# Kernel optimization log

Hardware: AMD Instinct MI355X
Metric: run time of the kernel (lower is better)

The kernel has to match this reference:

```python
import jax, jax.numpy as jnp
import numpy as np

N = 50000      # nodes
E = 800000     # edges (avg degree 16)
D = 128        # node_embedding_dim
H = 256        # hidden_dim


def setup_inputs() -> dict:
    key = jax.random.key(0)
    ks = jax.random.split(key, 12)
    init = lambda k, shape, fan: (jax.random.normal(k, shape, jnp.float32) / np.sqrt(fan).astype(np.float32))
    return {
        "node_ids": jnp.arange(N, dtype=jnp.int32),
        "edge_index": jax.random.randint(ks[0], (2, E), 0, N, jnp.int32),
        "neighbour_edge_index": jax.random.randint(ks[1], (2, E), 0, N, jnp.int32),
        "edge_attr": jax.random.uniform(ks[2], (E,), jnp.float32),
        "emb": init(ks[3], (N, D), D),          # Embedding table
        "W_in": init(ks[4], (D, H), D), "b_in": jnp.zeros((H,), jnp.float32),
        "W_out": init(ks[5], (H, D), H), "b_out": jnp.zeros((D,), jnp.float32),
        "W1": init(ks[6], (2 * D, D), 2 * D), "b1": jnp.zeros((D,), jnp.float32),
        "W2": init(ks[7], (D, D), D), "b2": jnp.zeros((D,), jnp.float32),
        "W3": init(ks[8], (D, 1), D), "b3": jnp.zeros((1,), jnp.float32),
    }


def gcn_conv(x, W, b, edge_index, w):
    """PyG GCNConv, add_self_loops=False, normalize=True.
    out_i = b + sum_{(j->i)} d_i^{-1/2} w_ji d_j^{-1/2} (x_j @ W)
    deg_i = sum of incoming edge weights at target node i.
    """
    row, col = edge_index[0], edge_index[1]
    deg = jax.ops.segment_sum(w, col, num_segments=N)
    dinv = jnp.where(deg > 0, 1.0 / jnp.sqrt(deg), 0.0)
    norm = dinv[row] * w * dinv[col]                    # [E]
    h = x @ W                                           # [N, out]
    msg = h[row] * norm[:, None]                        # [E, out]
    return jax.ops.segment_sum(msg, col, num_segments=N) + b


def reference(node_ids, edge_index, neighbour_edge_index, edge_attr,
              emb, W_in, b_in, W_out, b_out, W1, b1, W2, b2, W3, b3):
    x = emb[node_ids]                                   # embedding lookup [N, D]
    x = jax.nn.elu(gcn_conv(x, W_in, b_in, edge_index, edge_attr))
    ones = jnp.ones((neighbour_edge_index.shape[1],), x.dtype)
    x = jax.nn.elu(gcn_conv(x, W_out, b_out, neighbour_edge_index, ones))
    # edge-level gather-concat-MLP decoder
    src, dst = edge_index[0], edge_index[1]
    h = jnp.concatenate([x[src], x[dst]], axis=1)       # [E, 2D]
    h = jax.nn.relu(h @ W1 + b1)
    h = jax.nn.relu(h @ W2 + b2)
    return (h @ W3 + b3).squeeze(-1)                    # [E]
```

## Files before the change

kernel.cpp:

```cpp
#include <hip/hip_runtime.h>
#include <math.h>

#define NN 50000
#define NE 800000

typedef __attribute__((ext_vector_type(8))) short s8_t;
typedef __attribute__((ext_vector_type(4))) float f4_t;

__device__ __forceinline__ short bf16_rne(float v) {
  unsigned u = __float_as_uint(v);
  unsigned r = (u + 0x7FFFu + ((u >> 16) & 1u)) >> 16;
  return (short)r;
}
__device__ __forceinline__ float bf16_tof(short h) {
  return __uint_as_float(((unsigned)(unsigned short)h) << 16);
}
__device__ __forceinline__ void split2(float v, short& hi, short& lo) {
  hi = bf16_rne(v);
  lo = bf16_rne(v - bf16_tof(hi));
}


__global__ __launch_bounds__(256) void k_wcvt(const float* __restrict__ W1,
                                              const float* __restrict__ W2,
                                              short* __restrict__ w1th,
                                              short* __restrict__ w1tl,
                                              short* __restrict__ w2th,
                                              short* __restrict__ w2tl) {
  int i = blockIdx.x * 256 + threadIdx.x;
  if (i < 32768) {
    int k = i >> 7, n = i & 127;
    short h, l; split2(W1[i], h, l);
    w1th[n * 256 + k] = h; w1tl[n * 256 + k] = l;
  } else if (i < 49152) {
    int j = i - 32768;
    int k = j >> 7, n = j & 127;
    short h, l; split2(W2[j], h, l);
    w2th[n * 128 + k] = h; w2tl[n * 128 + k] = l;
  }
}


__global__ __launch_bounds__(256) void k_hist(const int* __restrict__ ei,
                                              const int* __restrict__ nei,
                                              const float* __restrict__ w,
                                              int* __restrict__ cnt1,
                                              float* __restrict__ deg1,
                                              int* __restrict__ cnt2) {
  int e = blockIdx.x * 256 + threadIdx.x;
  if (e < NE) {
    int c1 = ei[NE + e];
    atomicAdd(&cnt1[c1], 1);
    atomicAdd(&deg1[c1], w[e]);
    atomicAdd(&cnt2[nei[NE + e]], 1);
  }
}

__global__ __launch_bounds__(256) void k_dinvs(const float* __restrict__ deg1,
                                               const int* __restrict__ cnt2,
                                               float* __restrict__ dinv1,
                                               float* __restrict__ dinv2) {
  int i = blockIdx.x * 256 + threadIdx.x;
  if (i < NN) {
    float d1 = deg1[i];
    dinv1[i] = d1 > 0.f ? (1.0f / sqrtf(d1)) : 0.f;
    int c2 = cnt2[i];
    dinv2[i] = c2 > 0 ? (1.0f / sqrtf((float)c2)) : 0.f;
  }
}


#define NCHUNK 196

__global__ __launch_bounds__(256) void k_scan_part(const int* __restrict__ cnt1,
                                                   const int* __restrict__ cnt2,
                                                   int* __restrict__ part) {
  int g = blockIdx.x >= NCHUNK;
  int chunk = g ? blockIdx.x - NCHUNK : blockIdx.x;
  const int* cnt = g ? cnt2 : cnt1;
  int i = chunk * 256 + threadIdx.x;
  int v = (i < NN) ? cnt[i] : 0;
  __shared__ int sd[4];
#pragma unroll
  for (int o = 32; o; o >>= 1) v += __shfl_down(v, o);
  if ((threadIdx.x & 63) == 0) sd[threadIdx.x >> 6] = v;
  __syncthreads();
  if (threadIdx.x == 0) part[blockIdx.x] = sd[0] + sd[1] + sd[2] + sd[3];
}

__global__ __launch_bounds__(256) void k_scan_mid(int* __restrict__ part,
                                                  int* __restrict__ off1_last,
                                                  int* __restrict__ off2_last) {
  __shared__ int sd[256];
  for (int g = 0; g < 2; g++) {
    int base = g * NCHUNK;
    int v = (threadIdx.x < NCHUNK) ? part[base + threadIdx.x] : 0;
    sd[threadIdx.x] = v;
    __syncthreads();
    for (int o = 1; o < 256; o <<= 1) {
      int x = (threadIdx.x >= o) ? sd[threadIdx.x - o] : 0;
      __syncthreads();
      sd[threadIdx.x] += x;
      __syncthreads();
    }
    if (threadIdx.x < NCHUNK) part[base + threadIdx.x] = sd[threadIdx.x] - v;
    if (threadIdx.x == 255) *(g ? off2_last : off1_last) = sd[255];
    __syncthreads();
  }
}

__global__ __launch_bounds__(256) void k_scan_final(const int* __restrict__ cnt1,
                                                    const int* __restrict__ cnt2,
                                                    const int* __restrict__ part,
                                                    int* __restrict__ off1,
                                                    int* __restrict__ pos1,
                                                    int* __restrict__ off2,
                                                    int* __restrict__ pos2) {
  int g = blockIdx.x >= NCHUNK;
  int chunk = g ? blockIdx.x - NCHUNK : blockIdx.x;
  const int* cnt = g ? cnt2 : cnt1;
  int* off = g ? off2 : off1;
  int* pos = g ? pos2 : pos1;
  __shared__ int sd[256];
  int i = chunk * 256 + threadIdx.x;
  int v = (i < NN) ? cnt[i] : 0;
  sd[threadIdx.x] = v;
  __syncthreads();
  for (int o = 1; o < 256; o <<= 1) {
    int x = (threadIdx.x >= o) ? sd[threadIdx.x - o] : 0;
    __syncthreads();
    sd[threadIdx.x] += x;
    __syncthreads();
  }
  if (i < NN) {
    int ex = part[blockIdx.x] + sd[threadIdx.x] - v;
    off[i] = ex; pos[i] = ex;
  }
}


__global__ __launch_bounds__(256) void k_fill(const int* __restrict__ ei,
                                              const int* __restrict__ nei,
                                              const float* __restrict__ w,
                                              const float* __restrict__ dinv1,
                                              const float* __restrict__ dinv2,
                                              int* __restrict__ pos1,
                                              int* __restrict__ csr1_src,
                                              float* __restrict__ csr1_nrm,
                                              int* __restrict__ csr1_dst,
                                              int* __restrict__ csr1_eid,
                                              int* __restrict__ pos2,
                                              int* __restrict__ csr2_src,
                                              float* __restrict__ csr2_nrm) {
  int e = blockIdx.x * 256 + threadIdx.x;
  if (e < NE) {
    int r = ei[e], c = ei[NE + e];
    float nv = dinv1[r] * w[e] * dinv1[c];
    int s = atomicAdd(&pos1[c], 1);
    csr1_src[s] = r; csr1_nrm[s] = nv; csr1_dst[s] = c; csr1_eid[s] = e;
    int r2 = nei[e], c2 = nei[NE + e];
    float nv2 = dinv2[r2] * dinv2[c2];
    int s2 = atomicAdd(&pos2[c2], 1);
    csr2_src[s2] = r2; csr2_nrm[s2] = nv2;
  }
}


__global__ __launch_bounds__(256) void k_agg1(const int* __restrict__ off,
                                              const int* __restrict__ csr_src,
                                              const float* __restrict__ csr_nrm,
                                              const int* __restrict__ ids,
                                              const float* __restrict__ emb,
                                              float* __restrict__ aggX) {
  int wave = threadIdx.x >> 6, lane = threadIdx.x & 63;
  int node = blockIdx.x * 4 + wave;
  int start = off[node], end = off[node + 1];
  float2 acc = make_float2(0.f, 0.f);
  int i = start;
  for (; i + 3 < end; i += 4) {
    int s0 = csr_src[i], s1 = csr_src[i + 1], s2 = csr_src[i + 2], s3 = csr_src[i + 3];
    float n0 = csr_nrm[i], n1 = csr_nrm[i + 1], n2 = csr_nrm[i + 2], n3 = csr_nrm[i + 3];
    float2 v0 = *(const float2*)(emb + (size_t)ids[s0] * 128 + lane * 2);
    float2 v1 = *(const float2*)(emb + (size_t)ids[s1] * 128 + lane * 2);
    float2 v2 = *(const float2*)(emb + (size_t)ids[s2] * 128 + lane * 2);
    float2 v3 = *(const float2*)(emb + (size_t)ids[s3] * 128 + lane * 2);
    acc.x = fmaf(n0, v0.x, fmaf(n1, v1.x, fmaf(n2, v2.x, fmaf(n3, v3.x, acc.x))));
    acc.y = fmaf(n0, v0.y, fmaf(n1, v1.y, fmaf(n2, v2.y, fmaf(n3, v3.y, acc.y))));
  }
  for (; i < end; i++) {
    int s0 = csr_src[i];
    float n0 = csr_nrm[i];
    float2 v0 = *(const float2*)(emb + (size_t)ids[s0] * 128 + lane * 2);
    acc.x = fmaf(n0, v0.x, acc.x);
    acc.y = fmaf(n0, v0.y, acc.y);
  }
  *(float2*)(aggX + (size_t)node * 128 + lane * 2) = acc;
}


__global__ __launch_bounds__(256) void k_agg2(const int* __restrict__ off,
                                              const int* __restrict__ csr_src,
                                              const float* __restrict__ csr_nrm,
                                              const float* __restrict__ h2,
                                              const float* __restrict__ b,
                                              short* __restrict__ xh,
                                              short* __restrict__ xl) {
  int wave = threadIdx.x >> 6, lane = threadIdx.x & 63;
  int node = blockIdx.x * 4 + wave;
  int start = off[node], end = off[node + 1];
  float2 acc = make_float2(0.f, 0.f);
  int i = start;
  for (; i + 3 < end; i += 4) {
    int s0 = csr_src[i], s1 = csr_src[i + 1], s2 = csr_src[i + 2], s3 = csr_src[i + 3];
    float n0 = csr_nrm[i], n1 = csr_nrm[i + 1], n2 = csr_nrm[i + 2], n3 = csr_nrm[i + 3];
    float2 v0 = *(const float2*)(h2 + (size_t)s0 * 128 + lane * 2);
    float2 v1 = *(const float2*)(h2 + (size_t)s1 * 128 + lane * 2);
    float2 v2 = *(const float2*)(h2 + (size_t)s2 * 128 + lane * 2);
    float2 v3 = *(const float2*)(h2 + (size_t)s3 * 128 + lane * 2);
    acc.x = fmaf(n0, v0.x, fmaf(n1, v1.x, fmaf(n2, v2.x, fmaf(n3, v3.x, acc.x))));
    acc.y = fmaf(n0, v0.y, fmaf(n1, v1.y, fmaf(n2, v2.y, fmaf(n3, v3.y, acc.y))));
  }
  for (; i < end; i++) {
    int s0 = csr_src[i];
    float n0 = csr_nrm[i];
    float2 v0 = *(const float2*)(h2 + (size_t)s0 * 128 + lane * 2);
    acc.x = fmaf(n0, v0.x, acc.x);
    acc.y = fmaf(n0, v0.y, acc.y);
  }
  float vx = acc.x + b[lane * 2];
  float vy = acc.y + b[lane * 2 + 1];
  vx = vx > 0.f ? vx : expm1f(vx);
  vy = vy > 0.f ? vy : expm1f(vy);
  short hx, lx, hy, ly;
  split2(vx, hx, lx);
  split2(vy, hy, ly);
  unsigned hp = (unsigned)(unsigned short)hx | ((unsigned)(unsigned short)hy << 16);
  unsigned lp = (unsigned)(unsigned short)lx | ((unsigned)(unsigned short)ly << 16);
  *(unsigned*)(xh + (size_t)node * 128 + lane * 2) = hp;
  *(unsigned*)(xl + (size_t)node * 128 + lane * 2) = lp;
}


__global__ __launch_bounds__(256) void k_gemm_aggin(const float* __restrict__ X,
                                                    const float* __restrict__ W,
                                                    const float* __restrict__ b,
                                                    float* __restrict__ C) {
  __shared__ float As[32][128];
  int r0 = blockIdx.x * 32;
  int t = threadIdx.x;
  for (int i = t; i < 1024; i += 256) {
    int r = i >> 5, q = (i & 31) << 2;
    int rr = r0 + r;
    float4 v = make_float4(0.f, 0.f, 0.f, 0.f);
    if (rr < NN) v = *(const float4*)(X + (size_t)rr * 128 + q);
    *(float4*)(&As[r][q]) = v;
  }
  __syncthreads();
  int tc = t & 31, tr = t >> 5;
  int c0 = tc * 8, rr0 = tr * 4;
  float acc[4][8];
#pragma unroll
  for (int r = 0; r < 4; r++)
#pragma unroll
    for (int c = 0; c < 8; c++) acc[r][c] = 0.f;

  for (int k0 = 0; k0 < 128; k0 += 4) {
    float a_[4][4];
#pragma unroll
    for (int r = 0; r < 4; r++) {
      float4 v = *(const float4*)(&As[rr0 + r][k0]);
      a_[r][0] = v.x; a_[r][1] = v.y; a_[r][2] = v.z; a_[r][3] = v.w;
    }
#pragma unroll
    for (int kk = 0; kk < 4; kk++) {
      float4 w0 = *(const float4*)(W + (size_t)(k0 + kk) * 256 + c0);
      float4 w1 = *(const float4*)(W + (size_t)(k0 + kk) * 256 + c0 + 4);
#pragma unroll
      for (int r = 0; r < 4; r++) {
        float av = a_[r][kk];
        acc[r][0] += av * w0.x; acc[r][1] += av * w0.y;
        acc[r][2] += av * w0.z; acc[r][3] += av * w0.w;
        acc[r][4] += av * w1.x; acc[r][5] += av * w1.y;
        acc[r][6] += av * w1.z; acc[r][7] += av * w1.w;
      }
    }
  }
  float4 bb0 = *(const float4*)(b + c0);
  float4 bb1 = *(const float4*)(b + c0 + 4);
#pragma unroll
  for (int r = 0; r < 4; r++) {
    int rr = r0 + rr0 + r;
    if (rr < NN) {
      float o[8];
      o[0] = acc[r][0] + bb0.x; o[1] = acc[r][1] + bb0.y;
      o[2] = acc[r][2] + bb0.z; o[3] = acc[r][3] + bb0.w;
      o[4] = acc[r][4] + bb1.x; o[5] = acc[r][5] + bb1.y;
      o[6] = acc[r][6] + bb1.z; o[7] = acc[r][7] + bb1.w;
#pragma unroll
      for (int c = 0; c < 8; c++) o[c] = o[c] > 0.f ? o[c] : expm1f(o[c]);
      *(float4*)(C + (size_t)rr * 256 + c0) = make_float4(o[0], o[1], o[2], o[3]);
      *(float4*)(C + (size_t)rr * 256 + c0 + 4) = make_float4(o[4], o[5], o[6], o[7]);
    }
  }
}


__global__ __launch_bounds__(256) void k_gemm_mid(const float* __restrict__ X,
                                                  const float* __restrict__ W,
                                                  float* __restrict__ C) {
  __shared__ float As[32][256];
  int r0 = blockIdx.x * 32;
  int t = threadIdx.x;
  for (int i = t; i < 2048; i += 256) {
    int r = i >> 6, q = (i & 63) << 2;
    int rr = r0 + r;
    float4 v = make_float4(0.f, 0.f, 0.f, 0.f);
    if (rr < NN) v = *(const float4*)(X + (size_t)rr * 256 + q);
    *(float4*)(&As[r][q]) = v;
  }
  __syncthreads();
  int tc = t & 31, tr = t >> 5;
  int c0 = tc * 4, rr0 = tr * 4;
  float acc[4][4];
#pragma unroll
  for (int r = 0; r < 4; r++)
#pragma unroll
    for (int c = 0; c < 4; c++) acc[r][c] = 0.f;

  for (int k0 = 0; k0 < 256; k0 += 4) {
    float a_[4][4];
#pragma unroll
    for (int r = 0; r < 4; r++) {
      float4 v = *(const float4*)(&As[rr0 + r][k0]);
      a_[r][0] = v.x; a_[r][1] = v.y; a_[r][2] = v.z; a_[r][3] = v.w;
    }
#pragma unroll
    for (int kk = 0; kk < 4; kk++) {
      float4 w = *(const float4*)(W + (size_t)(k0 + kk) * 128 + c0);
#pragma unroll
      for (int r = 0; r < 4; r++) {
        float av = a_[r][kk];
        acc[r][0] += av * w.x; acc[r][1] += av * w.y;
        acc[r][2] += av * w.z; acc[r][3] += av * w.w;
      }
    }
  }
#pragma unroll
  for (int r = 0; r < 4; r++) {
    int rr = r0 + rr0 + r;
    if (rr < NN) {
      float4 o = make_float4(acc[r][0], acc[r][1], acc[r][2], acc[r][3]);
      *(float4*)(C + (size_t)rr * 128 + c0) = o;
    }
  }
}


__global__ __launch_bounds__(256) void k_pab(const short* __restrict__ x2h,
                                             const short* __restrict__ x2l,
                                             const short* __restrict__ w1th,
                                             const short* __restrict__ w1tl,
                                             const float* __restrict__ b1,
                                             float* __restrict__ Pa,
                                             float* __restrict__ Pb) {
  __shared__ short Xh[32 * 136];
  __shared__ short Xl[32 * 136];
  int t = threadIdx.x;
  int n0 = blockIdx.x * 32;
#pragma unroll
  for (int j = 0; j < 2; j++) {
    int i = t + 256 * j;
    int row = i >> 4, q = i & 15;
    int node = n0 + row; if (node >= NN) node = NN - 1;
    *(uint4*)&Xh[row * 136 + q * 8] = *(const uint4*)(x2h + (size_t)node * 128 + q * 8);
    *(uint4*)&Xl[row * 136 + q * 8] = *(const uint4*)(x2l + (size_t)node * 128 + q * 8);
  }
  __syncthreads();

  int w = t >> 6, lane = t & 63;
  int quad = lane >> 4, l16 = lane & 15;
  int nb = w * 32;
  int aoff0 = l16 * 136 + quad * 8;
  int aoff1 = (16 + l16) * 136 + quad * 8;
  int bo0 = (nb + l16) * 256 + quad * 8;
  int bo1 = (nb + 16 + l16) * 256 + quad * 8;

  f4_t aa[2][2], ab[2][2];
#pragma unroll
  for (int mi = 0; mi < 2; mi++)
#pragma unroll
    for (int ni = 0; ni < 2; ni++) {
      aa[mi][ni] = (f4_t){0.f, 0.f, 0.f, 0.f};
      ab[mi][ni] = (f4_t){0.f, 0.f, 0.f, 0.f};
    }

#pragma unroll
  for (int kb = 0; kb < 4; kb++) {
    int k0 = kb * 32;
    s8_t ah0 = *(const s8_t*)&Xh[aoff0 + k0];
    s8_t ah1 = *(const s8_t*)&Xh[aoff1 + k0];
    s8_t al0 = *(const s8_t*)&Xl[aoff0 + k0];
    s8_t al1 = *(const s8_t*)&Xl[aoff1 + k0];
    {
      s8_t bh0 = *(const s8_t*)(w1th + bo0 + k0);
      s8_t bh1 = *(const s8_t*)(w1th + bo1 + k0);
      s8_t bl0 = *(const s8_t*)(w1tl + bo0 + k0);
      s8_t bl1 = *(const s8_t*)(w1tl + bo1 + k0);
      aa[0][0] = __builtin_amdgcn_mfma_f32_16x16x32_bf16(ah0, bh0, aa[0][0], 0, 0, 0);
      aa[0][0] = __builtin_amdgcn_mfma_f32_16x16x32_bf16(ah0, bl0, aa[0][0], 0, 0, 0);
      aa[0][0] = __builtin_amdgcn_mfma_f32_16x16x32_bf16(al0, bh0, aa[0][0], 0, 0, 0);
      aa[0][1] = __builtin_amdgcn_mfma_f32_16x16x32_bf16(ah0, bh1, aa[0][1], 0, 0, 0);
      aa[0][1] = __builtin_amdgcn_mfma_f32_16x16x32_bf16(ah0, bl1, aa[0][1], 0, 0, 0);
      aa[0][1] = __builtin_amdgcn_mfma_f32_16x16x32_bf16(al0, bh1, aa[0][1], 0, 0, 0);
      aa[1][0] = __builtin_amdgcn_mfma_f32_16x16x32_bf16(ah1, bh0, aa[1][0], 0, 0, 0);
      aa[1][0] = __builtin_amdgcn_mfma_f32_16x16x32_bf16(ah1, bl0, aa[1][0], 0, 0, 0);
      aa[1][0] = __builtin_amdgcn_mfma_f32_16x16x32_bf16(al1, bh0, aa[1][0], 0, 0, 0);
      aa[1][1] = __builtin_amdgcn_mfma_f32_16x16x32_bf16(ah1, bh1, aa[1][1], 0, 0, 0);
      aa[1][1] = __builtin_amdgcn_mfma_f32_16x16x32_bf16(ah1, bl1, aa[1][1], 0, 0, 0);
      aa[1][1] = __builtin_amdgcn_mfma_f32_16x16x32_bf16(al1, bh1, aa[1][1], 0, 0, 0);
    }
    {
      s8_t bh0 = *(const s8_t*)(w1th + bo0 + 128 + k0);
      s8_t bh1 = *(const s8_t*)(w1th + bo1 + 128 + k0);
      s8_t bl0 = *(const s8_t*)(w1tl + bo0 + 128 + k0);
      s8_t bl1 = *(const s8_t*)(w1tl + bo1 + 128 + k0);
      ab[0][0] = __builtin_amdgcn_mfma_f32_16x16x32_bf16(ah0, bh0, ab[0][0], 0, 0, 0);
      ab[0][0] = __builtin_amdgcn_mfma_f32_16x16x32_bf16(ah0, bl0, ab[0][0], 0, 0, 0);
      ab[0][0] = __builtin_amdgcn_mfma_f32_16x16x32_bf16(al0, bh0, ab[0][0], 0, 0, 0);
      ab[0][1] = __builtin_amdgcn_mfma_f32_16x16x32_bf16(ah0, bh1, ab[0][1], 0, 0, 0);
      ab[0][1] = __builtin_amdgcn_mfma_f32_16x16x32_bf16(ah0, bl1, ab[0][1], 0, 0, 0);
      ab[0][1] = __builtin_amdgcn_mfma_f32_16x16x32_bf16(al0, bh1, ab[0][1], 0, 0, 0);
      ab[1][0] = __builtin_amdgcn_mfma_f32_16x16x32_bf16(ah1, bh0, ab[1][0], 0, 0, 0);
      ab[1][0] = __builtin_amdgcn_mfma_f32_16x16x32_bf16(ah1, bl0, ab[1][0], 0, 0, 0);
      ab[1][0] = __builtin_amdgcn_mfma_f32_16x16x32_bf16(al1, bh0, ab[1][0], 0, 0, 0);
      ab[1][1] = __builtin_amdgcn_mfma_f32_16x16x32_bf16(ah1, bh1, ab[1][1], 0, 0, 0);
      ab[1][1] = __builtin_amdgcn_mfma_f32_16x16x32_bf16(ah1, bl1, ab[1][1], 0, 0, 0);
      ab[1][1] = __builtin_amdgcn_mfma_f32_16x16x32_bf16(al1, bh1, ab[1][1], 0, 0, 0);
    }
  }

  float b1v0 = b1[nb + l16], b1v1 = b1[nb + 16 + l16];
#pragma unroll
  for (int mi = 0; mi < 2; mi++)
#pragma unroll
    for (int ni = 0; ni < 2; ni++) {
      int col = nb + ni * 16 + l16;
      float bv = ni ? b1v1 : b1v0;
#pragma unroll
      for (int r = 0; r < 4; r++) {
        int node = n0 + mi * 16 + quad * 4 + r;
        if (node < NN) {
          Pa[(size_t)node * 128 + col] = aa[mi][ni][r];
          Pb[(size_t)node * 128 + col] = ab[mi][ni][r] + bv;
        }
      }
    }
}


#define ST 136
#define S2 132

__global__ __launch_bounds__(256, 4) void k_decoder(
    const float* __restrict__ Pa, const float* __restrict__ Pb,
    const int* __restrict__ c1src, const int* __restrict__ c1dst,
    const int* __restrict__ c1eid,
    const short* __restrict__ w2th, const short* __restrict__ w2tl,
    const float* __restrict__ b2,
    const float* __restrict__ W3, const float* __restrict__ b3,
    float* __restrict__ out) {
  __shared__ short ThTl[2 * 32 * ST];
  short* Th = ThTl;
  short* Tl = ThTl + 32 * ST;
  float* T2 = (float*)ThTl;

  int t = threadIdx.x;
  int s0base = blockIdx.x * 32;

#pragma unroll
  for (int j = 0; j < 2; j++) {
    int i = t + 256 * j;
    int le = i >> 4, q = i & 15;
    int src = c1src[s0base + le], dst = c1dst[s0base + le];
    const float* pa = Pa + (size_t)src * 128 + q * 8;
    const float* pb = Pb + (size_t)dst * 128 + q * 8;
    float4 a0 = *(const float4*)(pa);
    float4 a1 = *(const float4*)(pa + 4);
    float4 c0 = *(const float4*)(pb);
    float4 c1 = *(const float4*)(pb + 4);
    float v[8];
    v[0] = a0.x + c0.x; v[1] = a0.y + c0.y;
    v[2] = a0.z + c0.z; v[3] = a0.w + c0.w;
    v[4] = a1.x + c1.x; v[5] = a1.y + c1.y;
    v[6] = a1.z + c1.z; v[7] = a1.w + c1.w;
    s8_t hv, lv;
#pragma unroll
    for (int k = 0; k < 8; k++) {
      float x = fmaxf(v[k], 0.f);
      short h, l; split2(x, h, l);
      hv[k] = h; lv[k] = l;
    }
    *(s8_t*)&Th[le * ST + q * 8] = hv;
    *(s8_t*)&Tl[le * ST + q * 8] = lv;
  }
  __syncthreads();

  int w = t >> 6, lane = t & 63;
  int quad = lane >> 4, l16 = lane & 15;
  int nb = w * 32;
  float b2v0 = b2[nb + l16], b2v1 = b2[nb + 16 + l16];
  float b3v = b3[0];

  int toff0 = l16 * ST + quad * 8;
  int toff1 = (16 + l16) * ST + quad * 8;
  int coff0 = (nb + l16) * 128 + quad * 8;
  int coff1 = (nb + 16 + l16) * 128 + quad * 8;

  f4_t acc2[2][2];
#pragma unroll
  for (int mi = 0; mi < 2; mi++)
#pragma unroll
    for (int ni = 0; ni < 2; ni++) acc2[mi][ni] = (f4_t){0.f, 0.f, 0.f, 0.f};

#pragma unroll
  for (int kb = 0; kb < 4; kb++) {
    int k0 = kb * 32;
    s8_t ah0 = *(const s8_t*)&Th[toff0 + k0];
    s8_t ah1 = *(const s8_t*)&Th[toff1 + k0];
    s8_t al0 = *(const s8_t*)&Tl[toff0 + k0];
    s8_t al1 = *(const s8_t*)&Tl[toff1 + k0];
    s8_t bh0 = *(const s8_t*)(w2th + coff0 + k0);
    s8_t bh1 = *(const s8_t*)(w2th + coff1 + k0);
    s8_t bl0 = *(const s8_t*)(w2tl + coff0 + k0);
    s8_t bl1 = *(const s8_t*)(w2tl + coff1 + k0);
    acc2[0][0] = __builtin_amdgcn_mfma_f32_16x16x32_bf16(ah0, bh0, acc2[0][0], 0, 0, 0);
    acc2[0][0] = __builtin_amdgcn_mfma_f32_16x16x32_bf16(ah0, bl0, acc2[0][0], 0, 0, 0);
    acc2[0][0] = __builtin_amdgcn_mfma_f32_16x16x32_bf16(al0, bh0, acc2[0][0], 0, 0, 0);
    acc2[0][1] = __builtin_amdgcn_mfma_f32_16x16x32_bf16(ah0, bh1, acc2[0][1], 0, 0, 0);
    acc2[0][1] = __builtin_amdgcn_mfma_f32_16x16x32_bf16(ah0, bl1, acc2[0][1], 0, 0, 0);
    acc2[0][1] = __builtin_amdgcn_mfma_f32_16x16x32_bf16(al0, bh1, acc2[0][1], 0, 0, 0);
    acc2[1][0] = __builtin_amdgcn_mfma_f32_16x16x32_bf16(ah1, bh0, acc2[1][0], 0, 0, 0);
    acc2[1][0] = __builtin_amdgcn_mfma_f32_16x16x32_bf16(ah1, bl0, acc2[1][0], 0, 0, 0);
    acc2[1][0] = __builtin_amdgcn_mfma_f32_16x16x32_bf16(al1, bh0, acc2[1][0], 0, 0, 0);
    acc2[1][1] = __builtin_amdgcn_mfma_f32_16x16x32_bf16(ah1, bh1, acc2[1][1], 0, 0, 0);
    acc2[1][1] = __builtin_amdgcn_mfma_f32_16x16x32_bf16(ah1, bl1, acc2[1][1], 0, 0, 0);
    acc2[1][1] = __builtin_amdgcn_mfma_f32_16x16x32_bf16(al1, bh1, acc2[1][1], 0, 0, 0);
  }
  __syncthreads();

#pragma unroll
  for (int mi = 0; mi < 2; mi++)
#pragma unroll
    for (int ni = 0; ni < 2; ni++) {
      float bv = ni ? b2v1 : b2v0;
      int col = nb + ni * 16 + l16;
#pragma unroll
      for (int r = 0; r < 4; r++) {
        int row = mi * 16 + quad * 4 + r;
        T2[row * S2 + col] = fmaxf(acc2[mi][ni][r] + bv, 0.f);
      }
    }
  __syncthreads();

  {
    int le = t >> 3, j0 = (t & 7) * 16;
    float s = 0.f;
#pragma unroll
    for (int j = 0; j < 16; j += 4) {
      float4 v = *(const float4*)(&T2[le * S2 + j0 + j]);
      float4 wv = *(const float4*)(W3 + j0 + j);
      s += v.x * wv.x + v.y * wv.y + v.z * wv.z + v.w * wv.w;
    }
    s += __shfl_down(s, 4);
    s += __shfl_down(s, 2);
    s += __shfl_down(s, 1);
    if ((t & 7) == 0) out[c1eid[s0base + le]] = s + b3v;
  }
}


extern "C" void kernel_launch(void* const* d_in, const int* in_sizes, int n_in,
                              void* d_out, int out_size, void* d_ws, size_t ws_size,
                              hipStream_t stream) {
  const int*   node_ids = (const int*)d_in[0];
  const int*   ei       = (const int*)d_in[1];
  const int*   nei      = (const int*)d_in[2];
  const float* eattr    = (const float*)d_in[3];
  const float* emb      = (const float*)d_in[4];
  const float* W_in     = (const float*)d_in[5];
  const float* b_in     = (const float*)d_in[6];
  const float* W_out    = (const float*)d_in[7];
  const float* b_out    = (const float*)d_in[8];
  const float* W1       = (const float*)d_in[9];
  const float* b1       = (const float*)d_in[10];
  const float* W2       = (const float*)d_in[11];
  const float* b2       = (const float*)d_in[12];
  const float* W3       = (const float*)d_in[13];
  const float* b3       = (const float*)d_in[14];
  float* out = (float*)d_out;

  float* ws    = (float*)d_ws;
  float* bufA  = ws;
  float* bufB  = bufA + (size_t)NN * 128;
  int*   cnt1  = (int*)(bufB + (size_t)NN * 256);
  int*   cnt2  = cnt1 + NN;
  float* deg1  = (float*)(cnt2 + NN);
  float* dinv1 = deg1 + NN;
  float* dinv2 = dinv1 + NN;
  int*   off1  = (int*)(dinv2 + NN);
  int*   pos1  = off1 + NN + 1;
  int*   off2  = pos1 + NN;
  int*   pos2  = off2 + NN + 1;
  int*   c1src = pos2 + NN;
  float* c1nrm = (float*)(c1src + NE);
  int*   c1dst = (int*)(c1nrm + NE);
  int*   c1eid = c1dst + NE;
  int*   c2src = c1eid + NE;
  float* c2nrm = (float*)(c2src + NE);
  short* w1th  = (short*)(c2nrm + NE);
  short* w1tl  = w1th + 32768;
  short* w2th  = w1tl + 32768;
  short* w2tl  = w2th + 16384;
  int*   part  = (int*)(w2tl + 16384);

  float* aggX  = bufA;
  float* h2    = bufA;
  float* Pa    = bufA;
  float* x1    = bufB;
  short* x2h   = (short*)bufB;
  short* x2l   = x2h + (size_t)NN * 128;
  float* Pb    = bufB + (size_t)NN * 128;

  k_wcvt<<<192, 256, 0, stream>>>(W1, W2, w1th, w1tl, w2th, w2tl);

  hipMemsetAsync(cnt1, 0, 3 * (size_t)NN * sizeof(int), stream);
  k_hist<<<NE / 256, 256, 0, stream>>>(ei, nei, eattr, cnt1, deg1, cnt2);
  k_dinvs<<<(NN + 255) / 256, 256, 0, stream>>>(deg1, cnt2, dinv1, dinv2);
  k_scan_part<<<2 * NCHUNK, 256, 0, stream>>>(cnt1, cnt2, part);
  k_scan_mid<<<1, 256, 0, stream>>>(part, off1 + NN, off2 + NN);
  k_scan_final<<<2 * NCHUNK, 256, 0, stream>>>(cnt1, cnt2, part,
                                               off1, pos1, off2, pos2);
  k_fill<<<NE / 256, 256, 0, stream>>>(ei, nei, eattr, dinv1, dinv2,
                                       pos1, c1src, c1nrm, c1dst, c1eid,
                                       pos2, c2src, c2nrm);

  k_agg1<<<NN / 4, 256, 0, stream>>>(off1, c1src, c1nrm, node_ids, emb, aggX);
  k_gemm_aggin<<<(NN + 31) / 32, 256, 0, stream>>>(aggX, W_in, b_in, x1);

  k_gemm_mid<<<(NN + 31) / 32, 256, 0, stream>>>(x1, W_out, h2);
  k_agg2<<<NN / 4, 256, 0, stream>>>(off2, c2src, c2nrm, h2, b_out, x2h, x2l);

  k_pab<<<(NN + 31) / 32, 256, 0, stream>>>(x2h, x2l, w1th, w1tl, b1, Pa, Pb);

  k_decoder<<<NE / 32, 256, 0, stream>>>(Pa, Pb, c1src, c1dst, c1eid,
                                         w2th, w2tl, b2, W3, b3, out);
}
```

Baseline: 829.1 us.

## Pack CSR arrays into structs, deepen gather unroll, fuse decoder final layer

Replaces the separate CSR arrays (src, norm, dst, eid) with packed int4/int2 records so each edge's metadata arrives in one vector load across fill, aggregation and decoder kernels. The aggregation loops are unrolled to 8 outstanding gathers to raise memory-level parallelism. The decoder now applies bias, ReLU and the W3 dot product directly on MFMA accumulators with shuffle reductions, which removes the shared-memory staging pass and one barrier. Decoder blocks are also remapped with a swizzled index (b&7)*3125+(b>>3) to change which edges run together. The int4 record adds padding bytes to loads where only some fields are needed.

```diff
diff --git a/kernel.cpp b/kernel.cpp
--- a/kernel.cpp
+++ b/kernel.cpp
@@ -145,30 +145,25 @@
                                               const float* __restrict__ dinv1,
                                               const float* __restrict__ dinv2,
                                               int* __restrict__ pos1,
-                                              int* __restrict__ csr1_src,
-                                              float* __restrict__ csr1_nrm,
-                                              int* __restrict__ csr1_dst,
-                                              int* __restrict__ csr1_eid,
+                                              int4* __restrict__ c1pack,
                                               int* __restrict__ pos2,
-                                              int* __restrict__ csr2_src,
-                                              float* __restrict__ csr2_nrm) {
+                                              int2* __restrict__ c2pack) {
   int e = blockIdx.x * 256 + threadIdx.x;
   if (e < NE) {
     int r = ei[e], c = ei[NE + e];
     float nv = dinv1[r] * w[e] * dinv1[c];
     int s = atomicAdd(&pos1[c], 1);
-    csr1_src[s] = r; csr1_nrm[s] = nv; csr1_dst[s] = c; csr1_eid[s] = e;
-    int r2 = nei[e], c2 = nei[NE + e];
-    float nv2 = dinv2[r2] * dinv2[c2];
-    int s2 = atomicAdd(&pos2[c2], 1);
-    csr2_src[s2] = r2; csr2_nrm[s2] = nv2;
+    c1pack[s] = make_int4(r, c, e, __float_as_int(nv));
+    int r2 = nei[e], c2v = nei[NE + e];
+    float nv2 = dinv2[r2] * dinv2[c2v];
+    int s2 = atomicAdd(&pos2[c2v], 1);
+    c2pack[s2] = make_int2(r2, __float_as_int(nv2));
   }
 }
 
 
 __global__ __launch_bounds__(256) void k_agg1(const int* __restrict__ off,
-                                              const int* __restrict__ csr_src,
-                                              const float* __restrict__ csr_nrm,
+                                              const int4* __restrict__ c1pack,
                                               const int* __restrict__ ids,
                                               const float* __restrict__ emb,
                                               float* __restrict__ aggX) {
@@ -177,20 +172,24 @@
   int start = off[node], end = off[node + 1];
   float2 acc = make_float2(0.f, 0.f);
   int i = start;
-  for (; i + 3 < end; i += 4) {
-    int s0 = csr_src[i], s1 = csr_src[i + 1], s2 = csr_src[i + 2], s3 = csr_src[i + 3];
-    float n0 = csr_nrm[i], n1 = csr_nrm[i + 1], n2 = csr_nrm[i + 2], n3 = csr_nrm[i + 3];
-    float2 v0 = *(const float2*)(emb + (size_t)ids[s0] * 128 + lane * 2);
-    float2 v1 = *(const float2*)(emb + (size_t)ids[s1] * 128 + lane * 2);
-    float2 v2 = *(const float2*)(emb + (size_t)ids[s2] * 128 + lane * 2);
-    float2 v3 = *(const float2*)(emb + (size_t)ids[s3] * 128 + lane * 2);
-    acc.x = fmaf(n0, v0.x, fmaf(n1, v1.x, fmaf(n2, v2.x, fmaf(n3, v3.x, acc.x))));
-    acc.y = fmaf(n0, v0.y, fmaf(n1, v1.y, fmaf(n2, v2.y, fmaf(n3, v3.y, acc.y))));
+  for (; i + 7 < end; i += 8) {
+    float2 v[8]; float n[8];
+#pragma unroll
+    for (int k = 0; k < 8; k++) {
+      int4 p = c1pack[i + k];
+      n[k] = __int_as_float(p.w);
+      v[k] = *(const float2*)(emb + (size_t)ids[p.x] * 128 + lane * 2);
+    }
+#pragma unroll
+    for (int k = 0; k < 8; k++) {
+      acc.x = fmaf(n[k], v[k].x, acc.x);
+      acc.y = fmaf(n[k], v[k].y, acc.y);
+    }
   }
   for (; i < end; i++) {
-    int s0 = csr_src[i];
-    float n0 = csr_nrm[i];
-    float2 v0 = *(const float2*)(emb + (size_t)ids[s0] * 128 + lane * 2);
+    int4 p = c1pack[i];
+    float n0 = __int_as_float(p.w);
+    float2 v0 = *(const float2*)(emb + (size_t)ids[p.x] * 128 + lane * 2);
     acc.x = fmaf(n0, v0.x, acc.x);
     acc.y = fmaf(n0, v0.y, acc.y);
   }
@@ -199,8 +198,7 @@
 
 
 __global__ __launch_bounds__(256) void k_agg2(const int* __restrict__ off,
-                                              const int* __restrict__ csr_src,
-                                              const float* __restrict__ csr_nrm,
+                                              const int2* __restrict__ c2pack,
                                               const float* __restrict__ h2,
                                               const float* __restrict__ b,
                                               short* __restrict__ xh,
@@ -210,20 +208,24 @@
   int start = off[node], end = off[node + 1];
   float2 acc = make_float2(0.f, 0.f);
   int i = start;
-  for (; i + 3 < end; i += 4) {
-    int s0 = csr_src[i], s1 = csr_src[i + 1], s2 = csr_src[i + 2], s3 = csr_src[i + 3];
-    float n0 = csr_nrm[i], n1 = csr_nrm[i + 1], n2 = csr_nrm[i + 2], n3 = csr_nrm[i + 3];
-    float2 v0 = *(const float2*)(h2 + (size_t)s0 * 128 + lane * 2);
-    float2 v1 = *(const float2*)(h2 + (size_t)s1 * 128 + lane * 2);
-    float2 v2 = *(const float2*)(h2 + (size_t)s2 * 128 + lane * 2);
-    float2 v3 = *(const float2*)(h2 + (size_t)s3 * 128 + lane * 2);
-    acc.x = fmaf(n0, v0.x, fmaf(n1, v1.x, fmaf(n2, v2.x, fmaf(n3, v3.x, acc.x))));
-    acc.y = fmaf(n0, v0.y, fmaf(n1, v1.y, fmaf(n2, v2.y, fmaf(n3, v3.y, acc.y))));
+  for (; i + 7 < end; i += 8) {
+    float2 v[8]; float n[8];
+#pragma unroll
+    for (int k = 0; k < 8; k++) {
+      int2 p = c2pack[i + k];
+      n[k] = __int_as_float(p.y);
+      v[k] = *(const float2*)(h2 + (size_t)p.x * 128 + lane * 2);
+    }
+#pragma unroll
+    for (int k = 0; k < 8; k++) {
+      acc.x = fmaf(n[k], v[k].x, acc.x);
+      acc.y = fmaf(n[k], v[k].y, acc.y);
+    }
   }
   for (; i < end; i++) {
-    int s0 = csr_src[i];
-    float n0 = csr_nrm[i];
-    float2 v0 = *(const float2*)(h2 + (size_t)s0 * 128 + lane * 2);
+    int2 p = c2pack[i];
+    float n0 = __int_as_float(p.y);
+    float2 v0 = *(const float2*)(h2 + (size_t)p.x * 128 + lane * 2);
     acc.x = fmaf(n0, v0.x, acc.x);
     acc.y = fmaf(n0, v0.y, acc.y);
   }
@@ -459,31 +461,30 @@
 
 
 #define ST 136
-#define S2 132
 
 __global__ __launch_bounds__(256, 4) void k_decoder(
     const float* __restrict__ Pa, const float* __restrict__ Pb,
-    const int* __restrict__ c1src, const int* __restrict__ c1dst,
-    const int* __restrict__ c1eid,
+    const int4* __restrict__ c1pack,
     const short* __restrict__ w2th, const short* __restrict__ w2tl,
     const float* __restrict__ b2,
     const float* __restrict__ W3, const float* __restrict__ b3,
     float* __restrict__ out) {
-  __shared__ short ThTl[2 * 32 * ST];
-  short* Th = ThTl;
-  short* Tl = ThTl + 32 * ST;
-  float* T2 = (float*)ThTl;
+  __shared__ short Th[32 * ST];
+  __shared__ short Tl[32 * ST];
+  __shared__ float part[4][32];
 
   int t = threadIdx.x;
-  int s0base = blockIdx.x * 32;
+  int b = blockIdx.x;
+  int id = (b & 7) * 3125 + (b >> 3);
+  int s0base = id * 32;
 
 #pragma unroll
   for (int j = 0; j < 2; j++) {
     int i = t + 256 * j;
     int le = i >> 4, q = i & 15;
-    int src = c1src[s0base + le], dst = c1dst[s0base + le];
-    const float* pa = Pa + (size_t)src * 128 + q * 8;
-    const float* pb = Pb + (size_t)dst * 128 + q * 8;
+    int4 p = c1pack[s0base + le];
+    const float* pa = Pa + (size_t)p.x * 128 + q * 8;
+    const float* pb = Pb + (size_t)p.y * 128 + q * 8;
     float4 a0 = *(const float4*)(pa);
     float4 a1 = *(const float4*)(pa + 4);
     float4 c0 = *(const float4*)(pb);
@@ -509,7 +510,7 @@
   int quad = lane >> 4, l16 = lane & 15;
   int nb = w * 32;
   float b2v0 = b2[nb + l16], b2v1 = b2[nb + 16 + l16];
-  float b3v = b3[0];
+  float w3a = W3[nb + l16], w3b = W3[nb + 16 + l16];
 
   int toff0 = l16 * ST + quad * 8;
   int toff1 = (16 + l16) * ST + quad * 8;
@@ -546,35 +547,26 @@
     acc2[1][1] = __builtin_amdgcn_mfma_f32_16x16x32_bf16(ah1, bl1, acc2[1][1], 0, 0, 0);
     acc2[1][1] = __builtin_amdgcn_mfma_f32_16x16x32_bf16(al1, bh1, acc2[1][1], 0, 0, 0);
   }
+
+#pragma unroll
+  for (int mi = 0; mi < 2; mi++) {
+#pragma unroll
+    for (int r = 0; r < 4; r++) {
+      float pv = fmaxf(acc2[mi][0][r] + b2v0, 0.f) * w3a +
+                 fmaxf(acc2[mi][1][r] + b2v1, 0.f) * w3b;
+      pv += __shfl_xor(pv, 1);
+      pv += __shfl_xor(pv, 2);
+      pv += __shfl_xor(pv, 4);
+      pv += __shfl_xor(pv, 8);
+      if (l16 == 0) part[w][mi * 16 + quad * 4 + r] = pv;
+    }
+  }
   __syncthreads();
 
-#pragma unroll
-  for (int mi = 0; mi < 2; mi++)
-#pragma unroll
-    for (int ni = 0; ni < 2; ni++) {
-      float bv = ni ? b2v1 : b2v0;
-      int col = nb + ni * 16 + l16;
-#pragma unroll
-      for (int r = 0; r < 4; r++) {
-        int row = mi * 16 + quad * 4 + r;
-        T2[row * S2 + col] = fmaxf(acc2[mi][ni][r] + bv, 0.f);
-      }
-    }
-  __syncthreads();
-
-  {
-    int le = t >> 3, j0 = (t & 7) * 16;
-    float s = 0.f;
-#pragma unroll
-    for (int j = 0; j < 16; j += 4) {
-      float4 v = *(const float4*)(&T2[le * S2 + j0 + j]);
-      float4 wv = *(const float4*)(W3 + j0 + j);
-      s += v.x * wv.x + v.y * wv.y + v.z * wv.z + v.w * wv.w;
-    }
-    s += __shfl_down(s, 4);
-    s += __shfl_down(s, 2);
-    s += __shfl_down(s, 1);
-    if ((t & 7) == 0) out[c1eid[s0base + le]] = s + b3v;
+  if (t < 32) {
+    float s = part[0][t] + part[1][t] + part[2][t] + part[3][t] + b3[0];
+    int4 p = c1pack[s0base + t];
+    out[p.z] = s;
   }
 }
 
@@ -611,13 +603,9 @@
   int*   pos1  = off1 + NN + 1;
   int*   off2  = pos1 + NN;
   int*   pos2  = off2 + NN + 1;
-  int*   c1src = pos2 + NN;
-  float* c1nrm = (float*)(c1src + NE);
-  int*   c1dst = (int*)(c1nrm + NE);
-  int*   c1eid = c1dst + NE;
-  int*   c2src = c1eid + NE;
-  float* c2nrm = (float*)(c2src + NE);
-  short* w1th  = (short*)(c2nrm + NE);
+  int4*  c1pack = (int4*)((((uintptr_t)(pos2 + NN)) + 15) & ~(uintptr_t)15);
+  int2*  c2pack = (int2*)(c1pack + NE);
+  short* w1th  = (short*)(c2pack + NE);
   short* w1tl  = w1th + 32768;
   short* w2th  = w1tl + 32768;
   short* w2tl  = w2th + 16384;
@@ -641,17 +629,16 @@
   k_scan_final<<<2 * NCHUNK, 256, 0, stream>>>(cnt1, cnt2, part,
                                                off1, pos1, off2, pos2);
   k_fill<<<NE / 256, 256, 0, stream>>>(ei, nei, eattr, dinv1, dinv2,
-                                       pos1, c1src, c1nrm, c1dst, c1eid,
-                                       pos2, c2src, c2nrm);
-
-  k_agg1<<<NN / 4, 256, 0, stream>>>(off1, c1src, c1nrm, node_ids, emb, aggX);
+                                       pos1, c1pack, pos2, c2pack);
+
+  k_agg1<<<NN / 4, 256, 0, stream>>>(off1, c1pack, node_ids, emb, aggX);
   k_gemm_aggin<<<(NN + 31) / 32, 256, 0, stream>>>(aggX, W_in, b_in, x1);
 
   k_gemm_mid<<<(NN + 31) / 32, 256, 0, stream>>>(x1, W_out, h2);
-  k_agg2<<<NN / 4, 256, 0, stream>>>(off2, c2src, c2nrm, h2, b_out, x2h, x2l);
+  k_agg2<<<NN / 4, 256, 0, stream>>>(off2, c2pack, h2, b_out, x2h, x2l);
 
   k_pab<<<(NN + 31) / 32, 256, 0, stream>>>(x2h, x2l, w1th, w1tl, b1, Pa, Pb);
 
-  k_decoder<<<NE / 32, 256, 0, stream>>>(Pa, Pb, c1src, c1dst, c1eid,
+  k_decoder<<<NE / 32, 256, 0, stream>>>(Pa, Pb, c1pack,
                                          w2th, w2tl, b2, W3, b3, out);
 }
```

Measured after the change: 806.6 us. -2.7%, faster.
